# Optimization experiments

Hardware: AMD Instinct MI355X
Metric: run time of the kernel (lower is better)

## Reference

```python
import jax, jax.numpy as jnp
import numpy as np

N = 50000      # nodes
E = 600000     # edges
D = 128        # in_channels
H = 128        # hidden_channels
C = 16         # out_channels
L = 3          # num GIN layers
G = 512        # graphs in batch
BN_EPS = 1e-5


def setup_inputs() -> dict:
    key = jax.random.key(0)
    ks = jax.random.split(key, 18)
    s = 0.05
    x = jax.random.normal(ks[0], (N, D), jnp.float32)
    edge_index = jax.random.randint(ks[1], (2, E), 0, N, dtype=jnp.int32)
    batch = jnp.sort(jax.random.randint(ks[2], (N,), 0, G, dtype=jnp.int32))
    # per-layer GIN MLP params (in_channels == hidden, so layers stack uniformly)
    W1s = jax.random.normal(ks[3], (L, D, H), jnp.float32) * s
    b1s = jnp.zeros((L, H), jnp.float32)
    g1s = jnp.ones((L, H), jnp.float32)    # inner BatchNorm gamma
    be1s = jnp.zeros((L, H), jnp.float32)  # inner BatchNorm beta
    W2s = jax.random.normal(ks[4], (L, H, H), jnp.float32) * s
    b2s = jnp.zeros((L, H), jnp.float32)
    gns = jnp.ones((L, H), jnp.float32)    # outer (post-conv) BatchNorm gamma
    bns = jnp.zeros((L, H), jnp.float32)
    # classifier head
    Wc1 = jax.random.normal(ks[5], (H, H), jnp.float32) * s
    bc1 = jnp.zeros((H,), jnp.float32)
    gc = jnp.ones((H,), jnp.float32)
    bec = jnp.zeros((H,), jnp.float32)
    Wc2 = jax.random.normal(ks[6], (H, C), jnp.float32) * s
    bc2 = jnp.zeros((C,), jnp.float32)
    return dict(x=x, edge_index=edge_index, batch=batch, W1s=W1s, b1s=b1s,
                g1s=g1s, be1s=be1s, W2s=W2s, b2s=b2s, gns=gns, bns=bns,
                Wc1=Wc1, bc1=bc1, gc=gc, bec=bec, Wc2=Wc2, bc2=bc2)


def _bn(h, gamma, beta):
    # BatchNorm1d in training mode: batch statistics over the node/row dim
    m = jnp.mean(h, axis=0)
    v = jnp.mean((h - m) ** 2, axis=0)
    return gamma * (h - m) * jax.lax.rsqrt(v + BN_EPS) + beta


def reference(x, edge_index, batch, W1s, b1s, g1s, be1s, W2s, b2s, gns, bns,
              Wc1, bc1, gc, bec, Wc2, bc2):
    src, dst = edge_index[0], edge_index[1]
    h = x
    for l in range(L):
        # GINConv, eps=0: mlp((1+eps)*x_i + sum_{j->i} x_j)
        agg = jax.ops.segment_sum(h[src], dst, num_segments=N) + h
        z = agg @ W1s[l] + b1s[l]
        z = jax.nn.relu(_bn(z, g1s[l], be1s[l]))
        z = z @ W2s[l] + b2s[l]
        h = jax.nn.relu(_bn(z, gns[l], bns[l]))
    # global mean pool over graphs
    counts = jax.ops.segment_sum(jnp.ones((N,), h.dtype), batch, num_segments=G)
    pooled = jax.ops.segment_sum(h, batch, num_segments=G) / jnp.maximum(counts, 1.0)[:, None]
    z = pooled @ Wc1 + bc1
    z = jax.nn.relu(_bn(z, gc, bec))
    return z @ Wc2 + bc2  # [G, C]
```

## Files before the change

### kernel.cpp

```cpp
#include <hip/hip_runtime.h>
#include <hip/hip_fp16.h>

#define NN 50000
#define NE 600000
#define DIM 128
#define NG 512
#define OC 16
#define BN_EPS 1e-5f

typedef __attribute__((ext_vector_type(8))) short short8v;
typedef __attribute__((ext_vector_type(8))) _Float16 half8v;
typedef __attribute__((ext_vector_type(2))) _Float16 h2v;
typedef __attribute__((ext_vector_type(4))) float f32x4;

__device__ inline float hbits2f(short s) {
    __half_raw hr; hr.x = (unsigned short)s;
    return __half2float(__half(hr));
}
__device__ inline short f2hbits(float f) {
    __half h = __float2half(f);
    short r;
    __builtin_memcpy(&r, &h, 2);
    return r;
}
__device__ inline h2v u2p(unsigned u) {
    h2v h;
    __builtin_memcpy(&h, &u, 4);
    return h;
}
__device__ inline unsigned p2u(h2v h) {
    unsigned u;
    __builtin_memcpy(&u, &h, 4);
    return u;
}
__device__ inline h2v f2p(float a, float b) {
    h2v h;
    h[0] = (_Float16)a;
    h[1] = (_Float16)b;
    return h;
}

__global__ void k_hist(const int* __restrict__ dst, int* __restrict__ deg, int e) {
    int i = blockIdx.x * blockDim.x + threadIdx.x;
    if (i < e) atomicAdd(&deg[dst[i]], 1);
}

__global__ void k_scan1(const int* __restrict__ deg, int* __restrict__ pre,
                        int* __restrict__ bsum, int n) {
    __shared__ int lds[1024];
    int t = threadIdx.x;
    int i = blockIdx.x * 1024 + t;
    int v = (i < n) ? deg[i] : 0;
    lds[t] = v;
    __syncthreads();
#pragma unroll
    for (int off = 1; off < 1024; off <<= 1) {
        int add = (t >= off) ? lds[t - off] : 0;
        __syncthreads();
        lds[t] += add;
        __syncthreads();
    }
    if (i < n) pre[i] = lds[t] - v;
    if (t == 1023) bsum[blockIdx.x] = lds[1023];
}

__global__ void k_scan3(const int* __restrict__ pre, const int* __restrict__ bsum,
                        const int* __restrict__ batch,
                        int* __restrict__ row_start, int* __restrict__ cursor,
                        int* __restrict__ gstart, int n, int nb) {
    __shared__ int boff[64];
    int t = threadIdx.x;
    if (t < 64) {
        int v = (t < nb) ? bsum[t] : 0;
        int orig = v;
#pragma unroll
        for (int off = 1; off < 64; off <<= 1) {
            int u = __shfl_up(v, off);
            if (t >= off) v += u;
        }
        boff[t] = v - orig;
    }
    __syncthreads();
    int i = blockIdx.x * blockDim.x + t;
    if (i < n) {
        int r = pre[i] + boff[i >> 10];
        row_start[i] = r;
        cursor[i] = r;
        int b = batch[i];
        int bp = (i == 0) ? -1 : batch[i - 1];
        for (int g = bp + 1; g <= b; g++) gstart[g] = i;
        if (i == n - 1) {
            for (int g = b + 1; g <= NG; g++) gstart[g] = n;
        }
    }
    if (i == 0) row_start[n] = NE;
}

__global__ void k_scatter(const int* __restrict__ src, const int* __restrict__ dst,
                          int* __restrict__ cursor, int* __restrict__ col, int e) {
    int i = blockIdx.x * blockDim.x + threadIdx.x;
    if (i < e) {
        int d = dst[i];
        int p = atomicAdd(&cursor[d], 1);
        col[p] = src[i];
    }
}

__global__ void k_transform0(const float* __restrict__ in, __half* __restrict__ out, int n4) {
    int i = blockIdx.x * blockDim.x + threadIdx.x;
    if (i >= n4) return;
    float4 v = ((const float4*)in)[i];
    uint2 pk;
    pk.x = p2u(f2p(v.x, v.y));
    pk.y = p2u(f2p(v.z, v.w));
    ((uint2*)out)[i] = pk;
}

template <int TRANSFORM>
__global__ void k_aggregate_q(const __half* __restrict__ Ht, const int* __restrict__ rs,
                              const int* __restrict__ col,
                              const float* __restrict__ stats, const float* __restrict__ gamma,
                              const float* __restrict__ beta, float invn,
                              __half* __restrict__ out, int n) {
    __shared__ float sst[256];
    int tid = threadIdx.x;
    if (TRANSFORM && tid < 128) {
        float s = stats[tid], q = stats[128 + tid];
        float m = s * invn;
        float var = fmaxf(q * invn - m * m, 0.f);
        float r = rsqrtf(var + BN_EPS);
        float sc = gamma[tid] * r;
        sst[tid] = sc;
        sst[128 + tid] = beta[tid] - m * sc;
    }
    if (TRANSFORM) __syncthreads();

    int node = blockIdx.x * 16 + (tid >> 4);
    if (node >= n) return;
    int ql = tid & 15;
    int c = ql * 8;
    h2v sc2[4], sh2[4];
    if (TRANSFORM) {
#pragma unroll
        for (int p = 0; p < 4; p++) {
            sc2[p] = f2p(sst[c + 2 * p], sst[c + 2 * p + 1]);
            sh2[p] = f2p(sst[128 + c + 2 * p], sst[129 + c + 2 * p]);
        }
    }
    const h2v zero2 = f2p(0.f, 0.f);
    const uint4* Hp = (const uint4*)Ht;

#define TRF2(H, P) (TRANSFORM ? __builtin_elementwise_max((H) * sc2[P] + sh2[P], zero2) : (H))
    h2v acc[4];
    {
        uint4 uv = Hp[(size_t)node * 16 + ql];
        acc[0] = TRF2(u2p(uv.x), 0);
        acc[1] = TRF2(u2p(uv.y), 1);
        acc[2] = TRF2(u2p(uv.z), 2);
        acc[3] = TRF2(u2p(uv.w), 3);
    }
    int s = rs[node], e = rs[node + 1];
    int i = s;
    for (; i + 3 < e; i += 4) {
        int j0 = col[i], j1 = col[i + 1], j2 = col[i + 2], j3 = col[i + 3];
        uint4 u0 = Hp[(size_t)j0 * 16 + ql];
        uint4 u1 = Hp[(size_t)j1 * 16 + ql];
        uint4 u2 = Hp[(size_t)j2 * 16 + ql];
        uint4 u3 = Hp[(size_t)j3 * 16 + ql];
        acc[0] += TRF2(u2p(u0.x), 0);
        acc[1] += TRF2(u2p(u0.y), 1);
        acc[2] += TRF2(u2p(u0.z), 2);
        acc[3] += TRF2(u2p(u0.w), 3);
        acc[0] += TRF2(u2p(u1.x), 0);
        acc[1] += TRF2(u2p(u1.y), 1);
        acc[2] += TRF2(u2p(u1.z), 2);
        acc[3] += TRF2(u2p(u1.w), 3);
        acc[0] += TRF2(u2p(u2.x), 0);
        acc[1] += TRF2(u2p(u2.y), 1);
        acc[2] += TRF2(u2p(u2.z), 2);
        acc[3] += TRF2(u2p(u2.w), 3);
        acc[0] += TRF2(u2p(u3.x), 0);
        acc[1] += TRF2(u2p(u3.y), 1);
        acc[2] += TRF2(u2p(u3.z), 2);
        acc[3] += TRF2(u2p(u3.w), 3);
    }
    for (; i < e; i++) {
        uint4 u0 = Hp[(size_t)col[i] * 16 + ql];
        acc[0] += TRF2(u2p(u0.x), 0);
        acc[1] += TRF2(u2p(u0.y), 1);
        acc[2] += TRF2(u2p(u0.z), 2);
        acc[3] += TRF2(u2p(u0.w), 3);
    }
#undef TRF2
    uint4 o;
    o.x = p2u(acc[0]);
    o.y = p2u(acc[1]);
    o.z = p2u(acc[2]);
    o.w = p2u(acc[3]);
    ((uint4*)out)[(size_t)node * 16 + ql] = o;
}

__global__ void k_prepw(const float* __restrict__ W1s, const float* __restrict__ W2s,
                        const float* __restrict__ Wc1, unsigned short* __restrict__ wfrag) {
    int idx = blockIdx.x * blockDim.x + threadIdx.x;
    if (idx >= 7 * 8 * 4 * 64) return;
    int lane = idx & 63;
    int k0 = (idx >> 6) & 3;
    int ct = (idx >> 8) & 7;
    int m = idx >> 11;
    const float* Wsrc = (m < 3) ? (W1s + (size_t)m * 16384)
                      : (m < 6) ? (W2s + (size_t)(m - 3) * 16384)
                                : Wc1;
    int colc = ct * 16 + (lane & 15);
    int kbase = k0 * 32 + (lane >> 4) * 8;
    short8v hi, lo;
#pragma unroll
    for (int j = 0; j < 8; j++) {
        float w = Wsrc[(size_t)(kbase + j) * 128 + colc];
        short hb = f2hbits(w);
        hi[j] = hb;
        lo[j] = f2hbits(w - hbits2f(hb));
    }
    size_t fo = ((size_t)(ct * 4 + k0) * 64 + lane) * 8;
    *(short8v*)(wfrag + (size_t)(m * 2 + 0) * 16384 + fo) = hi;
    *(short8v*)(wfrag + (size_t)(m * 2 + 1) * 16384 + fo) = lo;
}

#define MFMA16(A8, B8, C4) __builtin_amdgcn_mfma_f32_16x16x32_f16(A8, B8, C4, 0, 0, 0)

#define STORE_STATS(ACT, ACC0, ACC1, SUB)                                          \
    if (ACT) {                                                                     \
        int rowb = (SUB) * 16 + kb * 4;                                            \
        _Pragma("unroll")                                                          \
        for (int j = 0; j < 4; j++) {                                              \
            size_t i0 = (size_t)(rowb + j) * 128 + ct0 * 16 + rlo;                 \
            size_t i1 = (size_t)(rowb + j) * 128 + ct1 * 16 + rlo;                 \
            if (ZHALF) {                                                           \
                ((__half*)Zout)[i0] = __float2half(ACC0[j]);                       \
                ((__half*)Zout)[i1] = __float2half(ACC1[j]);                       \
            } else {                                                               \
                ((float*)Zout)[i0] = ACC0[j];                                      \
                ((float*)Zout)[i1] = ACC1[j];                                      \
            }                                                                      \
        }                                                                          \
        float s0 = ACC0[0] + ACC0[1] + ACC0[2] + ACC0[3];                          \
        float q0 = ACC0[0]*ACC0[0] + ACC0[1]*ACC0[1] + ACC0[2]*ACC0[2] + ACC0[3]*ACC0[3]; \
        float s1 = ACC1[0] + ACC1[1] + ACC1[2] + ACC1[3];                          \
        float q1 = ACC1[0]*ACC1[0] + ACC1[1]*ACC1[1] + ACC1[2]*ACC1[2] + ACC1[3]*ACC1[3]; \
        s0 += __shfl_xor(s0, 16); s0 += __shfl_xor(s0, 32);                        \
        q0 += __shfl_xor(q0, 16); q0 += __shfl_xor(q0, 32);                        \
        s1 += __shfl_xor(s1, 16); s1 += __shfl_xor(s1, 32);                        \
        q1 += __shfl_xor(q1, 16); q1 += __shfl_xor(q1, 32);                        \
        if (kb == 0) {                                                             \
            atomicAdd(&sred[ct0 * 16 + rlo], s0);                                  \
            atomicAdd(&sred[128 + ct0 * 16 + rlo], q0);                            \
            atomicAdd(&sred[ct1 * 16 + rlo], s1);                                  \
            atomicAdd(&sred[128 + ct1 * 16 + rlo], q1);                            \
        }                                                                          \
    }

template <int TRANSFORM, int ZHALF>
__global__ __launch_bounds__(256) void k_gemm_mfma(
        const __half* __restrict__ A, const unsigned short* __restrict__ wfragm,
        const float* __restrict__ bias,
        const float* __restrict__ statsIn, const float* __restrict__ gamma,
        const float* __restrict__ beta, float invn,
        void* __restrict__ Zout, float* __restrict__ statsOut, int nsub) {
    __shared__ short8v wldsHi[1024];
    __shared__ short8v wldsLo[1024];
    __shared__ float sred[256];
    __shared__ unsigned ssth[128];
    int tid = threadIdx.x;
    int wid = tid >> 6, lane = tid & 63;
    int sub0 = (blockIdx.x * 4 + wid) * 2;
    bool act0 = sub0 < nsub, act1 = sub0 + 1 < nsub;
    int rlo = lane & 15, kb = lane >> 4;

    sred[tid] = 0.f;
    if (TRANSFORM && tid < 64) {
        int c0 = tid * 2;
        float s0 = statsIn[c0], q0 = statsIn[128 + c0];
        float m0 = s0 * invn;
        float r0 = rsqrtf(fmaxf(q0 * invn - m0 * m0, 0.f) + BN_EPS);
        float sca = gamma[c0] * r0;
        float sha = beta[c0] - m0 * sca;
        float s1 = statsIn[c0 + 1], q1 = statsIn[129 + c0];
        float m1 = s1 * invn;
        float r1 = rsqrtf(fmaxf(q1 * invn - m1 * m1, 0.f) + BN_EPS);
        float scb = gamma[c0 + 1] * r1;
        float shb = beta[c0 + 1] - m1 * scb;
        ssth[tid] = p2u(f2p(sca, scb));
        ssth[64 + tid] = p2u(f2p(sha, shb));
    }
    __syncthreads();

    const h2v zero2 = f2p(0.f, 0.f);
    half8v af[2][4];
#pragma unroll
    for (int ss = 0; ss < 2; ss++) {
        bool act = ss ? act1 : act0;
        if (act) {
            const uint4* ap = (const uint4*)(A + ((size_t)(sub0 + ss) * 16 + rlo) * 128);
#pragma unroll
            for (int k0 = 0; k0 < 4; k0++) {
                uint4 uv = ap[k0 * 4 + kb];
                if (TRANSFORM) {
                    int hc = (k0 * 32 + kb * 8) >> 1;
                    uv.x = p2u(__builtin_elementwise_max(
                        u2p(uv.x) * u2p(ssth[hc + 0]) + u2p(ssth[64 + hc + 0]), zero2));
                    uv.y = p2u(__builtin_elementwise_max(
                        u2p(uv.y) * u2p(ssth[hc + 1]) + u2p(ssth[64 + hc + 1]), zero2));
                    uv.z = p2u(__builtin_elementwise_max(
                        u2p(uv.z) * u2p(ssth[hc + 2]) + u2p(ssth[64 + hc + 2]), zero2));
                    uv.w = p2u(__builtin_elementwise_max(
                        u2p(uv.w) * u2p(ssth[hc + 3]) + u2p(ssth[64 + hc + 3]), zero2));
                }
                __builtin_memcpy(&af[ss][k0], &uv, 16);
            }
        } else {
#pragma unroll
            for (int k0 = 0; k0 < 4; k0++) af[ss][k0] = half8v{0,0,0,0,0,0,0,0};
        }
    }

    const float4* wsrc = (const float4*)wfragm;
    float4* dH = (float4*)wldsHi;
    float4* dL = (float4*)wldsLo;

#pragma unroll
    for (int p = 0; p < 2; p++) {
        if (p) __syncthreads();
#pragma unroll
        for (int i = 0; i < 4; i++) {
            dH[tid + 256 * i] = wsrc[p * 1024 + tid + 256 * i];
            dL[tid + 256 * i] = wsrc[2048 + p * 1024 + tid + 256 * i];
        }
        __syncthreads();
#pragma unroll
        for (int cc = 0; cc < 2; cc++) {
            int ctp = 2 * p + cc;
            int ct0 = ctp * 2, ct1 = ct0 + 1;
            int l0 = ct0 - 4 * p, l1 = ct1 - 4 * p;
            float bb0 = bias[ct0 * 16 + rlo], bb1 = bias[ct1 * 16 + rlo];
            f32x4 acc00 = {bb0, bb0, bb0, bb0};
            f32x4 acc01 = {bb1, bb1, bb1, bb1};
            f32x4 acc10 = {bb0, bb0, bb0, bb0};
            f32x4 acc11 = {bb1, bb1, bb1, bb1};
#pragma unroll
            for (int k0 = 0; k0 < 4; k0++) {
                half8v bh0, bh1, bl0, bl1;
                __builtin_memcpy(&bh0, &wldsHi[(l0 * 4 + k0) * 64 + lane], 16);
                __builtin_memcpy(&bh1, &wldsHi[(l1 * 4 + k0) * 64 + lane], 16);
                __builtin_memcpy(&bl0, &wldsLo[(l0 * 4 + k0) * 64 + lane], 16);
                __builtin_memcpy(&bl1, &wldsLo[(l1 * 4 + k0) * 64 + lane], 16);
                acc00 = MFMA16(af[0][k0], bh0, acc00);
                acc10 = MFMA16(af[1][k0], bh0, acc10);
                acc01 = MFMA16(af[0][k0], bh1, acc01);
                acc11 = MFMA16(af[1][k0], bh1, acc11);
                acc00 = MFMA16(af[0][k0], bl0, acc00);
                acc10 = MFMA16(af[1][k0], bl0, acc10);
                acc01 = MFMA16(af[0][k0], bl1, acc01);
                acc11 = MFMA16(af[1][k0], bl1, acc11);
            }
            STORE_STATS(act0, acc00, acc01, sub0);
            STORE_STATS(act1, acc10, acc11, sub0 + 1);
        }
    }
    __syncthreads();
    if (tid < 128) {
        atomicAdd(&statsOut[tid], sred[tid]);
        atomicAdd(&statsOut[128 + tid], sred[128 + tid]);
    }
}

__global__ void k_pool_seg(const __half* __restrict__ H, const int* __restrict__ gstart,
                           const float* __restrict__ stats, const float* __restrict__ gamma,
                           const float* __restrict__ beta, float invn,
                           __half* __restrict__ out) {
    int g = blockIdx.x;
    int s = gstart[g], e = gstart[g + 1];
    int t = threadIdx.x;
    int lane = t & 63, wave = t >> 6;
    int c0 = lane * 2;
    float sc0, sc1, sh0, sh1;
    {
        float s0 = stats[c0], q0 = stats[128 + c0];
        float m0 = s0 * invn;
        float r0 = rsqrtf(fmaxf(q0 * invn - m0 * m0, 0.f) + BN_EPS);
        sc0 = gamma[c0] * r0; sh0 = beta[c0] - m0 * sc0;
        float s1 = stats[c0 + 1], q1 = stats[129 + c0];
        float m1 = s1 * invn;
        float r1 = rsqrtf(fmaxf(q1 * invn - m1 * m1, 0.f) + BN_EPS);
        sc1 = gamma[c0 + 1] * r1; sh1 = beta[c0 + 1] - m1 * sc1;
    }
    const __half2* Hp = (const __half2*)H;
    float ax = 0.f, ay = 0.f;
    for (int r = s + wave; r < e; r += 4) {
        float2 v = __half22float2(Hp[(size_t)r * 64 + lane]);
        ax += fmaxf(fmaf(v.x, sc0, sh0), 0.f);
        ay += fmaxf(fmaf(v.y, sc1, sh1), 0.f);
    }
    __shared__ float red[2][256];
    red[0][t] = ax;
    red[1][t] = ay;
    __syncthreads();
    if (wave == 0) {
        float inv = 1.f / fmaxf((float)(e - s), 1.f);
        float sx = red[0][lane] + red[0][64 + lane] + red[0][128 + lane] + red[0][192 + lane];
        float sy = red[1][lane] + red[1][64 + lane] + red[1][128 + lane] + red[1][192 + lane];
        ((__half2*)out)[g * 64 + lane] = __floats2half2_rn(sx * inv, sy * inv);
    }
}

__global__ void k_final(const float* __restrict__ Zh, const float* __restrict__ stats,
                        const float* __restrict__ gamma, const float* __restrict__ beta,
                        float invn, const float* __restrict__ Wc2,
                        const float* __restrict__ bc2, float* __restrict__ out) {
    __shared__ float Wl[128 * 16];
    __shared__ float Al[32 * 128];
    int tid = threadIdx.x;
    int kc = tid & 127;
    float s = stats[kc], q = stats[128 + kc];
    float m = s * invn;
    float rs = rsqrtf(fmaxf(q * invn - m * m, 0.f) + BN_EPS);
    float sck = gamma[kc] * rs;
    float shk = beta[kc] - m * sck;
#pragma unroll
    for (int i = 0; i < 4; i++) Wl[tid + 512 * i] = Wc2[tid + 512 * i];
#pragma unroll
    for (int i = 0; i < 8; i++) {
        int idx = tid + 512 * i;
        int gl = idx >> 7, k = idx & 127;
        float a = Zh[(size_t)(blockIdx.x * 32 + gl) * 128 + k];
        Al[idx] = fmaxf(fmaf(a, sck, shk), 0.f);
    }
    __syncthreads();
    int g = tid >> 4, c = tid & 15;
    float acc = bc2[c];
#pragma unroll 8
    for (int k = 0; k < 128; k++) acc = fmaf(Al[g * 128 + k], Wl[k * 16 + c], acc);
    out[(size_t)(blockIdx.x * 32 + g) * 16 + c] = acc;
}

extern "C" void kernel_launch(void* const* d_in, const int* in_sizes, int n_in,
                              void* d_out, int out_size, void* d_ws, size_t ws_size,
                              hipStream_t stream) {
    (void)in_sizes; (void)n_in; (void)out_size; (void)ws_size;
    const float* x    = (const float*)d_in[0];
    const int*   ei   = (const int*)d_in[1];
    const int*   srcv = ei;
    const int*   dstv = ei + NE;
    const int*   batch = (const int*)d_in[2];
    const float* W1s = (const float*)d_in[3];
    const float* b1s = (const float*)d_in[4];
    const float* g1s = (const float*)d_in[5];
    const float* be1s = (const float*)d_in[6];
    const float* W2s = (const float*)d_in[7];
    const float* b2s = (const float*)d_in[8];
    const float* gns = (const float*)d_in[9];
    const float* bns = (const float*)d_in[10];
    const float* Wc1 = (const float*)d_in[11];
    const float* bc1 = (const float*)d_in[12];
    const float* gc  = (const float*)d_in[13];
    const float* bec = (const float*)d_in[14];
    const float* Wc2 = (const float*)d_in[15];
    const float* bc2 = (const float*)d_in[16];
    float* out = (float*)d_out;

    char* ws = (char*)d_ws;
    size_t off = 0;
    auto alloc = [&](size_t bytes) -> char* {
        char* p = ws + off;
        off += (bytes + 255) & ~(size_t)255;
        return p;
    };
    int*   deg     = (int*)alloc(50048 * 4);
    float* statsZ  = (float*)alloc(7 * 256 * 4);
    size_t zeroBytes = off;
    int*   row_start = (int*)alloc((NN + 64) * 4);
    int*   cursor    = (int*)alloc((NN + 64) * 4);
    int*   pre       = (int*)alloc((NN + 64) * 4);
    int*   bsum      = (int*)alloc(64 * 4);
    int*   col       = (int*)alloc((NE + 64) * 4);
    int*   gstart    = (int*)alloc((NG + 1) * 4);
    unsigned short* wfrag = (unsigned short*)alloc((size_t)7 * 2 * 16384 * 2);
    __half* Ht     = (__half*)alloc((size_t)NN * 128 * 2);
    __half* aggH   = (__half*)alloc((size_t)NN * 128 * 2);
    __half* bufBh  = (__half*)alloc((size_t)NN * 128 * 2);
    __half* bufCh  = (__half*)alloc((size_t)NN * 128 * 2);
    __half* headAh = (__half*)alloc((size_t)NG * 128 * 2);
    float*  bufF   = (float*)alloc((size_t)NG * 128 * 4);

    hipMemsetAsync(d_ws, 0, zeroBytes, stream);

    k_prepw<<<56, 256, 0, stream>>>(W1s, W2s, Wc1, wfrag);

    k_hist<<<(NE + 255) / 256, 256, 0, stream>>>(dstv, deg, NE);
    int nb = (NN + 1023) / 1024;
    k_scan1<<<nb, 1024, 0, stream>>>(deg, pre, bsum, NN);
    k_scan3<<<(NN + 255) / 256, 256, 0, stream>>>(pre, bsum, batch, row_start, cursor,
                                                  gstart, NN, nb);
    k_scatter<<<(NE + 255) / 256, 256, 0, stream>>>(srcv, dstv, cursor, col, NE);

    int n4 = NN * 32;
    int tGrid = (n4 + 255) / 256;
    int aggGrid = NN / 16;
    int nsub = NN / 16;
    int gGrid = (nsub + 7) / 8;
    float invN = 1.f / NN;

    k_transform0<<<tGrid, 256, 0, stream>>>(x, Ht, n4);

    for (int l = 0; l < 3; l++) {
        float* s1 = statsZ + (size_t)(2 * l) * 256;
        float* s2 = statsZ + (size_t)(2 * l + 1) * 256;
        if (l == 0)
            k_aggregate_q<0><<<aggGrid, 256, 0, stream>>>(
                Ht, row_start, col, nullptr, nullptr, nullptr, 0.f, aggH, NN);
        else
            k_aggregate_q<1><<<aggGrid, 256, 0, stream>>>(
                bufCh, row_start, col, statsZ + (size_t)(2 * l - 1) * 256,
                gns + (l - 1) * 128, bns + (l - 1) * 128, invN, aggH, NN);
        k_gemm_mfma<0, 1><<<gGrid, 256, 0, stream>>>(
            aggH, wfrag + (size_t)(2 * l) * 16384, b1s + l * 128,
            nullptr, nullptr, nullptr, 0.f, bufBh, s1, nsub);
        k_gemm_mfma<1, 1><<<gGrid, 256, 0, stream>>>(
            bufBh, wfrag + (size_t)(2 * (3 + l)) * 16384, b2s + l * 128,
            s1, g1s + l * 128, be1s + l * 128, invN, bufCh, s2, nsub);
    }

    float* s2last = statsZ + (size_t)5 * 256;
    float* sHead  = statsZ + (size_t)6 * 256;
    k_pool_seg<<<NG, 256, 0, stream>>>(bufCh, gstart, s2last, gns + 2 * 128,
                                       bns + 2 * 128, invN, headAh);
    k_gemm_mfma<0, 0><<<4, 256, 0, stream>>>(
        headAh, wfrag + (size_t)12 * 16384, bc1,
        nullptr, nullptr, nullptr, 0.f, bufF, sHead, NG / 16);
    k_final<<<16, 512, 0, stream>>>(bufF, sHead, gc, bec, 1.f / NG, Wc2, bc2, out);
}
```

Before: 308.9 us.

## Fuse setup kernels into one launch and use 32 lanes per node in aggregation

Weight-fragment prep, the degree histogram and the fp32-to-fp16 input conversion now run as block ranges of a single setup kernel, which removes two launches. The aggregation kernel now gives each node 32 lanes with 8-byte loads instead of 16 lanes with 16-byte loads. It also keeps two independent accumulator pairs to shorten the add dependency chains. This trades wider per-node parallelism and more in-flight gathers for twice as many blocks and narrower memory transactions.

Measured after the change: 309.0 us. About the same (+0.0%).

```diff
diff --git a/kernel.cpp b/kernel.cpp
--- a/kernel.cpp
+++ b/kernel.cpp
@@ -40,9 +40,45 @@
     return h;
 }
 
-__global__ void k_hist(const int* __restrict__ dst, int* __restrict__ deg, int e) {
-    int i = blockIdx.x * blockDim.x + threadIdx.x;
-    if (i < e) atomicAdd(&deg[dst[i]], 1);
+__global__ void k_setup(const float* __restrict__ W1s, const float* __restrict__ W2s,
+                        const float* __restrict__ Wc1, unsigned short* __restrict__ wfrag,
+                        const int* __restrict__ dstv, int* __restrict__ deg,
+                        const float* __restrict__ x, __half* __restrict__ Ht) {
+    int b = blockIdx.x;
+    int t = threadIdx.x;
+    if (b < 56) {
+        int idx = b * 256 + t;
+        int lane = idx & 63;
+        int k0 = (idx >> 6) & 3;
+        int ct = (idx >> 8) & 7;
+        int m = idx >> 11;
+        const float* Wsrc = (m < 3) ? (W1s + (size_t)m * 16384)
+                          : (m < 6) ? (W2s + (size_t)(m - 3) * 16384)
+                                    : Wc1;
+        int colc = ct * 16 + (lane & 15);
+        int kbase = k0 * 32 + (lane >> 4) * 8;
+        short8v hi, lo;
+#pragma unroll
+        for (int j = 0; j < 8; j++) {
+            float w = Wsrc[(size_t)(kbase + j) * 128 + colc];
+            short hb = f2hbits(w);
+            hi[j] = hb;
+            lo[j] = f2hbits(w - hbits2f(hb));
+        }
+        size_t fo = ((size_t)(ct * 4 + k0) * 64 + lane) * 8;
+        *(short8v*)(wfrag + (size_t)(m * 2 + 0) * 16384 + fo) = hi;
+        *(short8v*)(wfrag + (size_t)(m * 2 + 1) * 16384 + fo) = lo;
+    } else if (b < 2400) {
+        int i = (b - 56) * 256 + t;
+        if (i < NE) atomicAdd(&deg[dstv[i]], 1);
+    } else {
+        int i = (b - 2400) * 256 + t;
+        float4 v = ((const float4*)x)[i];
+        uint2 pk;
+        pk.x = p2u(f2p(v.x, v.y));
+        pk.y = p2u(f2p(v.z, v.w));
+        ((uint2*)Ht)[i] = pk;
+    }
 }
 
 __global__ void k_scan1(const int* __restrict__ deg, int* __restrict__ pre,
@@ -106,18 +142,8 @@
     }
 }
 
-__global__ void k_transform0(const float* __restrict__ in, __half* __restrict__ out, int n4) {
-    int i = blockIdx.x * blockDim.x + threadIdx.x;
-    if (i >= n4) return;
-    float4 v = ((const float4*)in)[i];
-    uint2 pk;
-    pk.x = p2u(f2p(v.x, v.y));
-    pk.y = p2u(f2p(v.z, v.w));
-    ((uint2*)out)[i] = pk;
-}
-
 template <int TRANSFORM>
-__global__ void k_aggregate_q(const __half* __restrict__ Ht, const int* __restrict__ rs,
+__global__ void k_aggregate_h(const __half* __restrict__ Ht, const int* __restrict__ rs,
                               const int* __restrict__ col,
                               const float* __restrict__ stats, const float* __restrict__ gamma,
                               const float* __restrict__ beta, float invn,
@@ -135,95 +161,58 @@
     }
     if (TRANSFORM) __syncthreads();
 
-    int node = blockIdx.x * 16 + (tid >> 4);
+    int node = blockIdx.x * 8 + (tid >> 5);
     if (node >= n) return;
-    int ql = tid & 15;
-    int c = ql * 8;
-    h2v sc2[4], sh2[4];
+    int hl = tid & 31;
+    int c = hl * 4;
+    h2v sc2[2], sh2[2];
     if (TRANSFORM) {
-#pragma unroll
-        for (int p = 0; p < 4; p++) {
-            sc2[p] = f2p(sst[c + 2 * p], sst[c + 2 * p + 1]);
-            sh2[p] = f2p(sst[128 + c + 2 * p], sst[129 + c + 2 * p]);
-        }
+        sc2[0] = f2p(sst[c], sst[c + 1]);
+        sc2[1] = f2p(sst[c + 2], sst[c + 3]);
+        sh2[0] = f2p(sst[128 + c], sst[129 + c]);
+        sh2[1] = f2p(sst[130 + c], sst[131 + c]);
     }
     const h2v zero2 = f2p(0.f, 0.f);
-    const uint4* Hp = (const uint4*)Ht;
+    const uint2* Hp = (const uint2*)Ht;
 
 #define TRF2(H, P) (TRANSFORM ? __builtin_elementwise_max((H) * sc2[P] + sh2[P], zero2) : (H))
-    h2v acc[4];
+    h2v a0, a1, b0, b1;
     {
-        uint4 uv = Hp[(size_t)node * 16 + ql];
-        acc[0] = TRF2(u2p(uv.x), 0);
-        acc[1] = TRF2(u2p(uv.y), 1);
-        acc[2] = TRF2(u2p(uv.z), 2);
-        acc[3] = TRF2(u2p(uv.w), 3);
+        uint2 uv = Hp[(size_t)node * 32 + hl];
+        a0 = TRF2(u2p(uv.x), 0);
+        a1 = TRF2(u2p(uv.y), 1);
+        b0 = zero2;
+        b1 = zero2;
     }
     int s = rs[node], e = rs[node + 1];
     int i = s;
     for (; i + 3 < e; i += 4) {
         int j0 = col[i], j1 = col[i + 1], j2 = col[i + 2], j3 = col[i + 3];
-        uint4 u0 = Hp[(size_t)j0 * 16 + ql];
-        uint4 u1 = Hp[(size_t)j1 * 16 + ql];
-        uint4 u2 = Hp[(size_t)j2 * 16 + ql];
-        uint4 u3 = Hp[(size_t)j3 * 16 + ql];
-        acc[0] += TRF2(u2p(u0.x), 0);
-        acc[1] += TRF2(u2p(u0.y), 1);
-        acc[2] += TRF2(u2p(u0.z), 2);
-        acc[3] += TRF2(u2p(u0.w), 3);
-        acc[0] += TRF2(u2p(u1.x), 0);
-        acc[1] += TRF2(u2p(u1.y), 1);
-        acc[2] += TRF2(u2p(u1.z), 2);
-        acc[3] += TRF2(u2p(u1.w), 3);
-        acc[0] += TRF2(u2p(u2.x), 0);
-        acc[1] += TRF2(u2p(u2.y), 1);
-        acc[2] += TRF2(u2p(u2.z), 2);
-        acc[3] += TRF2(u2p(u2.w), 3);
-        acc[0] += TRF2(u2p(u3.x), 0);
-        acc[1] += TRF2(u2p(u3.y), 1);
-        acc[2] += TRF2(u2p(u3.z), 2);
-        acc[3] += TRF2(u2p(u3.w), 3);
+        uint2 u0 = Hp[(size_t)j0 * 32 + hl];
+        uint2 u1 = Hp[(size_t)j1 * 32 + hl];
+        uint2 u2e = Hp[(size_t)j2 * 32 + hl];
+        uint2 u3 = Hp[(size_t)j3 * 32 + hl];
+        a0 += TRF2(u2p(u0.x), 0);
+        a1 += TRF2(u2p(u0.y), 1);
+        b0 += TRF2(u2p(u1.x), 0);
+        b1 += TRF2(u2p(u1.y), 1);
+        a0 += TRF2(u2p(u2e.x), 0);
+        a1 += TRF2(u2p(u2e.y), 1);
+        b0 += TRF2(u2p(u3.x), 0);
+        b1 += TRF2(u2p(u3.y), 1);
     }
     for (; i < e; i++) {
-        uint4 u0 = Hp[(size_t)col[i] * 16 + ql];
-        acc[0] += TRF2(u2p(u0.x), 0);
-        acc[1] += TRF2(u2p(u0.y), 1);
-        acc[2] += TRF2(u2p(u0.z), 2);
-        acc[3] += TRF2(u2p(u0.w), 3);
+        uint2 u0 = Hp[(size_t)col[i] * 32 + hl];
+        b0 += TRF2(u2p(u0.x), 0);
+        b1 += TRF2(u2p(u0.y), 1);
     }
 #undef TRF2
-    uint4 o;
-    o.x = p2u(acc[0]);
-    o.y = p2u(acc[1]);
-    o.z = p2u(acc[2]);
-    o.w = p2u(acc[3]);
-    ((uint4*)out)[(size_t)node * 16 + ql] = o;
-}
-
-__global__ void k_prepw(const float* __restrict__ W1s, const float* __restrict__ W2s,
-                        const float* __restrict__ Wc1, unsigned short* __restrict__ wfrag) {
-    int idx = blockIdx.x * blockDim.x + threadIdx.x;
-    if (idx >= 7 * 8 * 4 * 64) return;
-    int lane = idx & 63;
-    int k0 = (idx >> 6) & 3;
-    int ct = (idx >> 8) & 7;
-    int m = idx >> 11;
-    const float* Wsrc = (m < 3) ? (W1s + (size_t)m * 16384)
-                      : (m < 6) ? (W2s + (size_t)(m - 3) * 16384)
-                                : Wc1;
-    int colc = ct * 16 + (lane & 15);
-    int kbase = k0 * 32 + (lane >> 4) * 8;
-    short8v hi, lo;
-#pragma unroll
-    for (int j = 0; j < 8; j++) {
-        float w = Wsrc[(size_t)(kbase + j) * 128 + colc];
-        short hb = f2hbits(w);
-        hi[j] = hb;
-        lo[j] = f2hbits(w - hbits2f(hb));
-    }
-    size_t fo = ((size_t)(ct * 4 + k0) * 64 + lane) * 8;
-    *(short8v*)(wfrag + (size_t)(m * 2 + 0) * 16384 + fo) = hi;
-    *(short8v*)(wfrag + (size_t)(m * 2 + 1) * 16384 + fo) = lo;
+    a0 += b0;
+    a1 += b1;
+    uint2 o;
+    o.x = p2u(a0);
+    o.y = p2u(a1);
+    ((uint2*)out)[(size_t)node * 32 + hl] = o;
 }
 
 #define MFMA16(A8, B8, C4) __builtin_amdgcn_mfma_f32_16x16x32_f16(A8, B8, C4, 0, 0, 0)
@@ -493,32 +482,27 @@
 
     hipMemsetAsync(d_ws, 0, zeroBytes, stream);
 
-    k_prepw<<<56, 256, 0, stream>>>(W1s, W2s, Wc1, wfrag);
-
-    k_hist<<<(NE + 255) / 256, 256, 0, stream>>>(dstv, deg, NE);
+    k_setup<<<8650, 256, 0, stream>>>(W1s, W2s, Wc1, wfrag, dstv, deg, x, Ht);
+
     int nb = (NN + 1023) / 1024;
     k_scan1<<<nb, 1024, 0, stream>>>(deg, pre, bsum, NN);
     k_scan3<<<(NN + 255) / 256, 256, 0, stream>>>(pre, bsum, batch, row_start, cursor,
                                                   gstart, NN, nb);
     k_scatter<<<(NE + 255) / 256, 256, 0, stream>>>(srcv, dstv, cursor, col, NE);
 
-    int n4 = NN * 32;
-    int tGrid = (n4 + 255) / 256;
-    int aggGrid = NN / 16;
+    int aggGrid = NN / 8;
     int nsub = NN / 16;
     int gGrid = (nsub + 7) / 8;
     float invN = 1.f / NN;
-
-    k_transform0<<<tGrid, 256, 0, stream>>>(x, Ht, n4);
 
     for (int l = 0; l < 3; l++) {
         float* s1 = statsZ + (size_t)(2 * l) * 256;
         float* s2 = statsZ + (size_t)(2 * l + 1) * 256;
         if (l == 0)
-            k_aggregate_q<0><<<aggGrid, 256, 0, stream>>>(
+            k_aggregate_h<0><<<aggGrid, 256, 0, stream>>>(
                 Ht, row_start, col, nullptr, nullptr, nullptr, 0.f, aggH, NN);
         else
-            k_aggregate_q<1><<<aggGrid, 256, 0, stream>>>(
+            k_aggregate_h<1><<<aggGrid, 256, 0, stream>>>(
                 bufCh, row_start, col, statsZ + (size_t)(2 * l - 1) * 256,
                 gns + (l - 1) * 128, bns + (l - 1) * 128, invN, aggH, NN);
         k_gemm_mfma<0, 1><<<gGrid, 256, 0, stream>>>(
```
